# Optimization experiments

Measured on AMD Instinct MI355X. Metric: run time of the kernel, lower is better.

Reference implementation:

```python
import jax, jax.numpy as jnp
import numpy as np

N_EMBD = 1024
N_HEAD = 16
EPS = 1e-5


def setup_inputs() -> dict:
    key = jax.random.key(0)
    ks = jax.random.split(key, 12)
    C = N_EMBD
    s = 1.0 / np.sqrt(C)
    s4 = 1.0 / np.sqrt(4 * C)
    return {
        "x": jax.random.normal(ks[0], (2, 2048, C), jnp.float32),
        # attention projections (stored as [in, out])
        "wq": jax.random.normal(ks[1], (C, C), jnp.float32) * s,
        "bq": jnp.zeros((C,), jnp.float32),
        "wk": jax.random.normal(ks[2], (C, C), jnp.float32) * s,
        "bk": jnp.zeros((C,), jnp.float32),
        "wv": jax.random.normal(ks[3], (C, C), jnp.float32) * s,
        "bv": jnp.zeros((C,), jnp.float32),
        # layernorms
        "ln1_w": jnp.ones((C,), jnp.float32),
        "ln1_b": jnp.zeros((C,), jnp.float32),
        "ln2_w": jnp.ones((C,), jnp.float32),
        "ln2_b": jnp.zeros((C,), jnp.float32),
        # MLP
        "w_fc": jax.random.normal(ks[4], (C, 4 * C), jnp.float32) * s,
        "b_fc": jnp.zeros((4 * C,), jnp.float32),
        "w_proj": jax.random.normal(ks[5], (4 * C, C), jnp.float32) * s4,
        "b_proj": jnp.zeros((C,), jnp.float32),
    }


def _layer_norm(x, w, b):
    mu = jnp.mean(x, axis=-1, keepdims=True)
    var = jnp.var(x, axis=-1, keepdims=True)
    return (x - mu) * jax.lax.rsqrt(var + EPS) * w + b


def _block(x, wq, bq, wk, bk, wv, bv, ln1_w, ln1_b, ln2_w, ln2_b,
           w_fc, b_fc, w_proj, b_proj):
    B, T, C = x.shape
    H, D = N_HEAD, C // N_HEAD
    h = _layer_norm(x, ln1_w, ln1_b)
    q = (h @ wq + bq).reshape(B, T, H, D).transpose(0, 2, 1, 3)  # [B,H,T,D]
    k = (h @ wk + bk).reshape(B, T, H, D).transpose(0, 2, 1, 3)
    v = (h @ wv + bv).reshape(B, T, H, D).transpose(0, 2, 1, 3)
    att = jnp.einsum("bhtd,bhsd->bhts", q, k) / np.sqrt(D)
    causal = jnp.tril(jnp.ones((T, T), bool))
    att = jnp.where(causal, att, -jnp.inf)
    att = jax.nn.softmax(att, axis=-1)
    y = jnp.einsum("bhts,bhsd->bhtd", att, v)
    y = y.transpose(0, 2, 1, 3).reshape(B, T, C)
    x = x + y
    h2 = _layer_norm(x, ln2_w, ln2_b)
    mlp = jax.nn.gelu(h2 @ w_fc + b_fc, approximate=False) @ w_proj + b_proj
    x = x + mlp
    return x, k, v


def reference(x, wq, bq, wk, bk, wv, bv, ln1_w, ln1_b, ln2_w, ln2_b,
              w_fc, b_fc, w_proj, b_proj):
    return _block(x, wq, bq, wk, bk, wv, bv, ln1_w, ln1_b, ln2_w, ln2_b,
                  w_fc, b_fc, w_proj, b_proj)
```

## Files before the change

### kernel.cpp

```cpp
#include <hip/hip_runtime.h>
#include <hip/hip_bf16.h>


#define T_SEQ 2048
#define C_DIM 1024
#define HEADS 16
#define HD    64

typedef __attribute__((ext_vector_type(8))) short s16x8;
typedef __attribute__((ext_vector_type(4))) short s16x4;
typedef __attribute__((ext_vector_type(4))) float f32x4;

__device__ __forceinline__ short f2bf(float f) {
    union { __hip_bfloat16 h; short s; } u;
    u.h = __float2bfloat16(f);
    return u.s;
}
__device__ __forceinline__ float bf2f(short s) {
    union { float f; unsigned u; } u;
    u.u = ((unsigned)(unsigned short)s) << 16;
    return u.f;
}

__device__ __forceinline__ void gload16(const void* g, void* l) {
    __builtin_amdgcn_global_load_lds(
        (const __attribute__((address_space(1))) void*)g,
        (__attribute__((address_space(3))) void*)l, 16, 0, 0);
}
#define VMCNT0 asm volatile("s_waitcnt vmcnt(0)" ::: "memory")
#define PRIO1  __builtin_amdgcn_s_setprio(1)
#define PRIO0  __builtin_amdgcn_s_setprio(0)

__global__ __launch_bounds__(256) void prep_kernel(
    const float* __restrict__ wq, const float* __restrict__ wk, const float* __restrict__ wv,
    const float* __restrict__ wfc, const float* __restrict__ wpr,
    short* __restrict__ wqkvt, short* __restrict__ wfct, short* __restrict__ wprt,
    const float* __restrict__ x, const float* __restrict__ ln1w, const float* __restrict__ ln1b,
    short* __restrict__ hb) {
    int b = blockIdx.x, tid = threadIdx.x;
    if (b < 11264) {
        const float* W; short* Wt; int K, N, n0, k0;
        if (b < 3072) {
            int which = b >> 10, sub = b & 1023;
            W = (which == 0) ? wq : ((which == 1) ? wk : wv);
            Wt = wqkvt + which * 1024 * 1024;
            K = 1024; N = 1024;
            n0 = (sub & 31) * 32; k0 = (sub >> 5) * 32;
        } else if (b < 7168) {
            int sub = b - 3072;
            W = wfc; Wt = wfct; K = 1024; N = 4096;
            n0 = (sub & 127) * 32; k0 = (sub >> 7) * 32;
        } else {
            int sub = b - 7168;
            W = wpr; Wt = wprt; K = 4096; N = 1024;
            n0 = (sub & 31) * 32; k0 = (sub >> 5) * 32;
        }
        __shared__ float t[32][33];
        int ty = tid >> 3, tx = tid & 7;
        float4 v = *(const float4*)&W[(size_t)(k0 + ty) * N + n0 + tx * 4];
        t[ty][tx * 4 + 0] = v.x; t[ty][tx * 4 + 1] = v.y;
        t[ty][tx * 4 + 2] = v.z; t[ty][tx * 4 + 3] = v.w;
        __syncthreads();
        int r = tid >> 3, c = tid & 7;
        s16x4 o;
#pragma unroll
        for (int j = 0; j < 4; j++) o[j] = f2bf(t[c * 4 + j][r]);
        *(s16x4*)&Wt[(size_t)(n0 + r) * K + k0 + c * 4] = o;
    } else {
        int row = b - 11264;
        float4 v = ((const float4*)(x + (size_t)row * C_DIM))[tid];
        float s  = v.x + v.y + v.z + v.w;
        float sq = v.x * v.x + v.y * v.y + v.z * v.z + v.w * v.w;
#pragma unroll
        for (int off = 32; off > 0; off >>= 1) {
            s  += __shfl_down(s, off, 64);
            sq += __shfl_down(sq, off, 64);
        }
        __shared__ float rs[4], rq[4];
        int wv2 = tid >> 6, ln = tid & 63;
        if (ln == 0) { rs[wv2] = s; rq[wv2] = sq; }
        __syncthreads();
        s = rs[0] + rs[1] + rs[2] + rs[3];
        sq = rq[0] + rq[1] + rq[2] + rq[3];
        float mean = s * (1.f / C_DIM);
        float rstd = rsqrtf(sq * (1.f / C_DIM) - mean * mean + 1e-5f);
        float4 wv4 = ((const float4*)ln1w)[tid];
        float4 bv4 = ((const float4*)ln1b)[tid];
        s16x4 o;
        o[0] = f2bf((v.x - mean) * rstd * wv4.x + bv4.x);
        o[1] = f2bf((v.y - mean) * rstd * wv4.y + bv4.y);
        o[2] = f2bf((v.z - mean) * rstd * wv4.z + bv4.z);
        o[3] = f2bf((v.w - mean) * rstd * wv4.w + bv4.w);
        *(s16x4*)(hb + (size_t)row * C_DIM + tid * 4) = o;
    }
}

__global__ __launch_bounds__(256) void resln_kernel(
    const float* __restrict__ x, const float* __restrict__ y,
    const float* __restrict__ w, const float* __restrict__ b,
    const float* __restrict__ bproj,
    short* __restrict__ out, float* __restrict__ xout) {
    int row = blockIdx.x, tid = threadIdx.x;
    float4 vx = ((const float4*)(x + row * C_DIM))[tid];
    float4 vy = ((const float4*)(y + row * C_DIM))[tid];
    float4 v;
    v.x = vx.x + vy.x; v.y = vx.y + vy.y; v.z = vx.z + vy.z; v.w = vx.w + vy.w;
    float4 bp = ((const float4*)bproj)[tid];
    float4 xo;
    xo.x = v.x + bp.x; xo.y = v.y + bp.y; xo.z = v.z + bp.z; xo.w = v.w + bp.w;
    ((float4*)(xout + row * C_DIM))[tid] = xo;
    float s  = v.x + v.y + v.z + v.w;
    float sq = v.x * v.x + v.y * v.y + v.z * v.z + v.w * v.w;
#pragma unroll
    for (int off = 32; off > 0; off >>= 1) {
        s  += __shfl_down(s, off, 64);
        sq += __shfl_down(sq, off, 64);
    }
    __shared__ float rs[4], rq[4];
    int wv = tid >> 6, ln = tid & 63;
    if (ln == 0) { rs[wv] = s; rq[wv] = sq; }
    __syncthreads();
    s = rs[0] + rs[1] + rs[2] + rs[3];
    sq = rq[0] + rq[1] + rq[2] + rq[3];
    float mean = s * (1.f / C_DIM);
    float rstd = rsqrtf(sq * (1.f / C_DIM) - mean * mean + 1e-5f);
    float4 wv4 = ((const float4*)w)[tid];
    float4 bv4 = ((const float4*)b)[tid];
    s16x4 o;
    o[0] = f2bf((v.x - mean) * rstd * wv4.x + bv4.x);
    o[1] = f2bf((v.y - mean) * rstd * wv4.y + bv4.y);
    o[2] = f2bf((v.z - mean) * rstd * wv4.z + bv4.z);
    o[3] = f2bf((v.w - mean) * rstd * wv4.w + bv4.w);
    *(s16x4*)(out + row * C_DIM + tid * 4) = o;
}

__global__ __launch_bounds__(256) void reduce_kernel(
    const short* __restrict__ p, float* __restrict__ xout) {
    size_t i = (size_t)blockIdx.x * 256 + threadIdx.x;
    float4 a = ((const float4*)xout)[i];
#pragma unroll
    for (int c = 0; c < 4; c++) {
        s16x4 v = ((const s16x4*)(p + (size_t)c * 4194304))[i];
        a.x += bf2f(v[0]); a.y += bf2f(v[1]); a.z += bf2f(v[2]); a.w += bf2f(v[3]);
    }
    ((float4*)xout)[i] = a;
}

template<int MODE>
__global__ __launch_bounds__(512, 1) void gemm2p(
    const short* __restrict__ A, const short* __restrict__ Bt,
    int K, int LDA, int N,
    const float* __restrict__ b0, const float* __restrict__ b1, const float* __restrict__ b2,
    short* __restrict__ os0, short* __restrict__ os1, short* __restrict__ os2,
    float* __restrict__ of0) {
    constexpr int MFR = 8, NFR = 4;

    __shared__ short As[2][256 * 64];
    __shared__ short Bs[2][256 * 64];

    const int tid = threadIdx.x;
    const int wv = tid >> 6, lane = tid & 63, g = lane >> 4, r4 = lane & 15;
    const int wm = wv >> 2, wn = wv & 3;
    const int lr = lane >> 3, lc = lane & 7, sc = lc ^ lr;

    const int nwg = gridDim.x * gridDim.y;
    const int bid = blockIdx.y * gridDim.x + blockIdx.x;
    const int swz = (bid & 7) * (nwg >> 3) + (bid >> 3);
    const int m0 = (swz % gridDim.x) * 256;
    const int yy = swz / gridDim.x;
    int n0, kch;
    if constexpr (MODE == 2) {
        kch = yy >> 2;
        n0 = (yy & 3) * 256;
    } else {
        kch = 0;
        n0 = yy * 256;
    }
    const size_t kbase = (size_t)kch * K;
    const size_t aoff = (size_t)m0 * LDA + kbase + sc * 8;
    const size_t boff = (size_t)n0 * LDA + kbase + sc * 8;

    const f32x4 zero4 = {0.f, 0.f, 0.f, 0.f};
    f32x4 acc[MFR][NFR];
#pragma unroll
    for (int i = 0; i < MFR; i++)
#pragma unroll
        for (int j = 0; j < NFR; j++) acc[i][j] = zero4;

    auto stage = [&](int bb, int t1) {
#pragma unroll
        for (int j = 0; j < 4; j++) {
            int rbase = j * 64 + wv * 8;
            gload16(A  + aoff + (size_t)(rbase + lr) * LDA + (size_t)t1 * 64, &As[bb][rbase * 64]);
            gload16(Bt + boff + (size_t)(rbase + lr) * LDA + (size_t)t1 * 64, &Bs[bb][rbase * 64]);
        }
    };

    stage(0, 0);
    __syncthreads();

    const int NT = K >> 6;
    int cur = 0;
    for (int t = 0; t < NT; ++t) {
        if (t + 1 < NT) stage(cur ^ 1, t + 1);
        const char* Ac = (const char*)&As[cur][0];
        const char* Bc = (const char*)&Bs[cur][0];
#pragma unroll
        for (int kk = 0; kk < 2; kk++) {
            s16x8 aF[MFR], bF[NFR];
#pragma unroll
            for (int mf = 0; mf < MFR; mf++) {
                int row = wm * 128 + mf * 16 + r4;
                aF[mf] = *(const s16x8*)(Ac + ((row * 128 + kk * 64 + g * 16) ^ ((row & 7) << 4)));
            }
#pragma unroll
            for (int nf = 0; nf < NFR; nf++) {
                int row = wn * 64 + nf * 16 + r4;
                bF[nf] = *(const s16x8*)(Bc + ((row * 128 + kk * 64 + g * 16) ^ ((row & 7) << 4)));
            }
            PRIO1;
#pragma unroll
            for (int mf = 0; mf < MFR; mf++)
#pragma unroll
                for (int nf = 0; nf < NFR; nf++)
                    acc[mf][nf] = __builtin_amdgcn_mfma_f32_16x16x32_bf16(
                        aF[mf], bF[nf], acc[mf][nf], 0, 0, 0);
            PRIO0;
        }
        __syncthreads();
        cur ^= 1;
    }

#pragma unroll
    for (int mf = 0; mf < MFR; mf++) {
#pragma unroll
        for (int nf = 0; nf < NFR; nf++) {
            int n = n0 + wn * 64 + nf * 16 + r4;
            int mB = m0 + wm * 128 + mf * 16 + 4 * g;
            if constexpr (MODE == 0) {
                int sel = n >> 10, nn = n & 1023;
                const float* bp = (sel == 0) ? b0 : ((sel == 1) ? b1 : b2);
                float bias = bp[nn];
                int h = nn >> 6, d = nn & 63;
                int bb2 = mB >> 11, tt = mB & 2047;
                size_t qz = ((size_t)(bb2 * HEADS + h) * T_SEQ + tt) * HD + d;
                if (sel == 0) {
#pragma unroll
                    for (int r = 0; r < 4; r++)
                        os0[qz + (size_t)r * HD] = f2bf((acc[mf][nf][r] + bias) * 0.18033688f);
                } else if (sel == 1) {
#pragma unroll
                    for (int r = 0; r < 4; r++) {
                        float val = acc[mf][nf][r] + bias;
                        os1[qz + (size_t)r * HD] = f2bf(val);
                        of0[qz + (size_t)r * HD] = val;
                    }
                } else {
                    s16x4 vp;
#pragma unroll
                    for (int r = 0; r < 4; r++) {
                        float val = acc[mf][nf][r] + bias;
                        of0[4194304 + qz + (size_t)r * HD] = val;
                        vp[r] = f2bf(val);
                    }
                    *(s16x4*)&os2[((size_t)(bb2 * HEADS + h) * HD + d) * T_SEQ + tt] = vp;
                }
            } else if constexpr (MODE == 1) {
                float bias = b0[n];
#pragma unroll
                for (int r = 0; r < 4; r++) {
                    float val = acc[mf][nf][r] + bias;
                    float u = val * (0.7978845608f + 0.0356774081f * val * val);
                    float e = exp2f(fminf(u * 2.885390082f, 126.f));
                    val = val * e * (1.f / 1.f + 0.f);
                    val = (acc[mf][nf][r] + bias);
                    u = val * (0.7978845608f + 0.0356774081f * val * val);
                    e = exp2f(fminf(u * 2.885390082f, 126.f));
                    val = val * (e / (e + 1.f));
                    os0[(size_t)(mB + r) * N + n] = f2bf(val);
                }
            } else {
#pragma unroll
                for (int r = 0; r < 4; r++)
                    os0[(size_t)kch * 4194304 + (size_t)(mB + r) * N + n] = f2bf(acc[mf][nf][r]);
            }
        }
    }
}

__global__ __launch_bounds__(512) void attn_kernel(
    const short* __restrict__ qb, const short* __restrict__ kb,
    const short* __restrict__ vtb, float* __restrict__ y) {
    __shared__ short Ks[2][2][64 * 64];
    __shared__ short Vs[2][2][64 * 64];
    __shared__ short Ps[8][32 * 64];
    __shared__ float MLb[4][2][16][2];
    float* Ymrg = (float*)&Ps[0][0];

    int bx = blockIdx.x, bh = blockIdx.y;
    int tid = threadIdx.x, w = tid >> 6, lane = tid & 63, g = lane >> 4, r4 = lane & 15;
    int wq = w & 3, g2 = w >> 2;
    int lr = lane >> 3, lc = lane & 7, sc = lc ^ lr;
    const f32x4 zero4 = {0.f, 0.f, 0.f, 0.f};

    for (int ph = 0; ph < 2; ++ph) {
        int qtr = ph ? bx : (15 - bx);
        int qbase = qtr * 128;

        const short* Qp = qb + ((size_t)bh * T_SEQ + qbase + wq * 32 + r4) * HD;
        s16x8 qf[2][2];
        qf[0][0] = *(const s16x8*)&Qp[g * 8];
        qf[0][1] = *(const s16x8*)&Qp[32 + g * 8];
        qf[1][0] = *(const s16x8*)&Qp[16 * HD + g * 8];
        qf[1][1] = *(const s16x8*)&Qp[16 * HD + 32 + g * 8];

        f32x4 yacc[2][4];
#pragma unroll
        for (int qh = 0; qh < 2; qh++)
#pragma unroll
            for (int ni = 0; ni < 4; ni++) yacc[qh][ni] = zero4;
        float mrun[2] = {-1e30f, -1e30f}, lrun[2] = {0.f, 0.f};

#pragma unroll
        for (int j = 0; j < 2; j++) {
            int rw = (wq * 2 + j) * 8 + lr;
            gload16(kb  + ((size_t)bh * T_SEQ + g2 * 64 + rw) * HD + sc * 8,
                    &Ks[g2][0][(wq * 2 + j) * 512]);
            gload16(vtb + ((size_t)bh * HD + rw) * T_SEQ + g2 * 64 + sc * 8,
                    &Vs[g2][0][(wq * 2 + j) * 512]);
        }
        VMCNT0;
        __syncthreads();

        for (int i = 0; i <= qtr; ++i) {
            int cur = i & 1;
            int s0 = (2 * i + g2) * 64;
            if (i + 1 <= qtr) {
#pragma unroll
                for (int j = 0; j < 2; j++) {
                    int rw = (wq * 2 + j) * 8 + lr;
                    gload16(kb  + ((size_t)bh * T_SEQ + s0 + 128 + rw) * HD + sc * 8,
                            &Ks[g2][cur ^ 1][(wq * 2 + j) * 512]);
                    gload16(vtb + ((size_t)bh * HD + rw) * T_SEQ + s0 + 128 + sc * 8,
                            &Vs[g2][cur ^ 1][(wq * 2 + j) * 512]);
                }
            }
            f32x4 sacc[2][4];
#pragma unroll
            for (int qh = 0; qh < 2; qh++)
#pragma unroll
                for (int sb = 0; sb < 4; sb++) sacc[qh][sb] = zero4;
            PRIO1;
#pragma unroll
            for (int kk = 0; kk < 2; kk++) {
#pragma unroll
                for (int sb = 0; sb < 4; sb++) {
                    int srow = sb * 16 + r4;
                    s16x8 kf = *(const s16x8*)((const char*)&Ks[g2][cur][0] +
                                ((srow * 128 + kk * 64 + g * 16) ^ ((r4 & 7) << 4)));
                    sacc[0][sb] = __builtin_amdgcn_mfma_f32_16x16x32_bf16(kf, qf[0][kk], sacc[0][sb], 0, 0, 0);
                    sacc[1][sb] = __builtin_amdgcn_mfma_f32_16x16x32_bf16(kf, qf[1][kk], sacc[1][sb], 0, 0, 0);
                }
            }
            PRIO0;
            bool diag = (i == qtr);
            float p[2][4][4];
#pragma unroll
            for (int qh = 0; qh < 2; qh++) {
                float mx = -3e38f;
#pragma unroll
                for (int sb = 0; sb < 4; sb++)
#pragma unroll
                    for (int r = 0; r < 4; r++) {
                        float v = sacc[qh][sb][r];
                        if (diag) {
                            int kv = s0 + sb * 16 + 4 * g + r;
                            int qg = qbase + wq * 32 + qh * 16 + r4;
                            if (kv > qg) v = -3e38f;
                        }
                        p[qh][sb][r] = v;
                        mx = fmaxf(mx, v);
                    }
                mx = fmaxf(mx, __shfl_xor(mx, 16, 64));
                mx = fmaxf(mx, __shfl_xor(mx, 32, 64));
                if (!__all(mx <= mrun[qh] + 8.f)) {
                    float mnew = fmaxf(mrun[qh], mx);
                    float alpha = exp2f(mrun[qh] - mnew);
                    float aC[4];
#pragma unroll
                    for (int r = 0; r < 4; r++) aC[r] = __shfl(alpha, 4 * g + r, 64);
#pragma unroll
                    for (int ni = 0; ni < 4; ni++)
#pragma unroll
                        for (int r = 0; r < 4; r++) yacc[qh][ni][r] *= aC[r];
                    lrun[qh] *= alpha;
                    mrun[qh] = mnew;
                }
                float rsum = 0.f;
#pragma unroll
                for (int sb = 0; sb < 4; sb++)
#pragma unroll
                    for (int r = 0; r < 4; r++) {
                        float e = exp2f(p[qh][sb][r] - mrun[qh]);
                        p[qh][sb][r] = e;
                        rsum += e;
                    }
                rsum += __shfl_xor(rsum, 16, 64);
                rsum += __shfl_xor(rsum, 32, 64);
                lrun[qh] += rsum;
#pragma unroll
                for (int sb = 0; sb < 4; sb++) {
                    s16x4 pk;
#pragma unroll
                    for (int r = 0; r < 4; r++) pk[r] = f2bf(p[qh][sb][r]);
                    int off = (((qh * 16 + r4) * 128) + (sb * 16 + 4 * g) * 2) ^ ((r4 & 7) << 4);
                    *(s16x4*)((char*)&Ps[w][0] + off) = pk;
                }
            }
            PRIO1;
#pragma unroll
            for (int kk = 0; kk < 2; kk++) {
                s16x8 pf[2];
#pragma unroll
                for (int qh = 0; qh < 2; qh++)
                    pf[qh] = *(const s16x8*)((const char*)&Ps[w][0] +
                              ((((qh * 16 + r4) * 128) + kk * 64 + g * 16) ^ ((r4 & 7) << 4)));
#pragma unroll
                for (int ni = 0; ni < 4; ni++) {
                    int vrow = ni * 16 + r4;
                    s16x8 vb = *(const s16x8*)((const char*)&Vs[g2][cur][0] +
                                ((vrow * 128 + kk * 64 + g * 16) ^ ((r4 & 7) << 4)));
                    yacc[0][ni] = __builtin_amdgcn_mfma_f32_16x16x32_bf16(pf[0], vb, yacc[0][ni], 0, 0, 0);
                    yacc[1][ni] = __builtin_amdgcn_mfma_f32_16x16x32_bf16(pf[1], vb, yacc[1][ni], 0, 0, 0);
                }
            }
            PRIO0;
            VMCNT0;
            __syncthreads();
        }
        if (g2 == 1) {
            if (g == 0) {
#pragma unroll
                for (int qh = 0; qh < 2; qh++) {
                    MLb[wq][qh][r4][0] = mrun[qh];
                    MLb[wq][qh][r4][1] = lrun[qh];
                }
            }
#pragma unroll
            for (int qh = 0; qh < 2; qh++)
#pragma unroll
                for (int ni = 0; ni < 4; ni++)
#pragma unroll
                    for (int r = 0; r < 4; r++)
                        Ymrg[wq * 2048 + (qh * 16 + 4 * g + r) * 64 + ni * 16 + r4] = yacc[qh][ni][r];
        }
        __syncthreads();
        if (g2 == 0) {
            int bb = bh >> 4, h = bh & 15;
#pragma unroll
            for (int qh = 0; qh < 2; qh++) {
                float m_b = MLb[wq][qh][r4][0], l_b = MLb[wq][qh][r4][1];
                float mM = fmaxf(mrun[qh], m_b);
                float fa = exp2f(mrun[qh] - mM), fb = exp2f(m_b - mM);
                float lM = lrun[qh] * fa + l_b * fb;
                float faC[4], fbC[4], lC[4];
#pragma unroll
                for (int r = 0; r < 4; r++) {
                    faC[r] = __shfl(fa, 4 * g + r, 64);
                    fbC[r] = __shfl(fb, 4 * g + r, 64);
                    lC[r]  = __shfl(lM, 4 * g + r, 64);
                }
#pragma unroll
                for (int ni = 0; ni < 4; ni++)
#pragma unroll
                    for (int r = 0; r < 4; r++) {
                        float yv = yacc[qh][ni][r] * faC[r] +
                                   Ymrg[wq * 2048 + (qh * 16 + 4 * g + r) * 64 + ni * 16 + r4] * fbC[r];
                        int q = qbase + wq * 32 + qh * 16 + 4 * g + r;
                        y[((size_t)bb * T_SEQ + q) * C_DIM + h * HD + ni * 16 + r4] = yv / lC[r];
                    }
            }
        }
        __syncthreads();
    }
}

extern "C" void kernel_launch(void* const* d_in, const int* in_sizes, int n_in,
                              void* d_out, int out_size, void* d_ws, size_t ws_size,
                              hipStream_t stream) {
    (void)in_sizes; (void)n_in; (void)out_size; (void)ws_size;
    const float* x    = (const float*)d_in[0];
    const float* wq   = (const float*)d_in[1];
    const float* bq   = (const float*)d_in[2];
    const float* wk   = (const float*)d_in[3];
    const float* bk   = (const float*)d_in[4];
    const float* wvp  = (const float*)d_in[5];
    const float* bv   = (const float*)d_in[6];
    const float* ln1w = (const float*)d_in[7];
    const float* ln1b = (const float*)d_in[8];
    const float* ln2w = (const float*)d_in[9];
    const float* ln2b = (const float*)d_in[10];
    const float* wfc  = (const float*)d_in[11];
    const float* bfc  = (const float*)d_in[12];
    const float* wpr  = (const float*)d_in[13];
    const float* bpr  = (const float*)d_in[14];

    float* xout = (float*)d_out;
    float* kout = xout + 4194304;

    short* wqkvt = (short*)d_ws;
    short* wfct  = wqkvt + 3072 * 1024;
    short* wprt  = wfct + 4096 * 1024;
    short* hb    = wprt + 1024 * 4096;
    short* qb    = hb + 4096 * 1024;
    short* kbuf  = qb + 4096 * 1024;
    short* vtb   = kbuf + 4096 * 1024;
    short* h2b   = vtb + 4096 * 1024;
    short* fcb   = h2b + 4096 * 1024;
    float* ybuf  = (float*)(fcb + 4096 * 4096);
    short* pbuf  = qb;

    prep_kernel<<<15360, 256, 0, stream>>>(wq, wk, wvp, wfc, wpr,
        wqkvt, wfct, wprt, x, ln1w, ln1b, hb);

    gemm2p<0><<<dim3(16, 12), 512, 0, stream>>>(hb, wqkvt, 1024, 1024, 3072,
        bq, bk, bv, qb, kbuf, vtb, kout);

    attn_kernel<<<dim3(8, 32), 512, 0, stream>>>(qb, kbuf, vtb, ybuf);

    resln_kernel<<<4096, 256, 0, stream>>>(x, ybuf, ln2w, ln2b, bpr, h2b, xout);

    gemm2p<1><<<dim3(16, 16), 512, 0, stream>>>(h2b, wfct, 1024, 1024, 4096,
        bfc, nullptr, nullptr, fcb, nullptr, nullptr, nullptr);

    gemm2p<2><<<dim3(16, 16), 512, 0, stream>>>(fcb, wprt, 1024, 4096, 1024,
        nullptr, nullptr, nullptr, pbuf, nullptr, nullptr, nullptr);

    reduce_kernel<<<4096, 256, 0, stream>>>(pbuf, xout);
}
```

Before: 227.6 us.

## Single-buffer V tile and drop redundant GELU recomputation in MLP epilogue

In the attention kernel, V tiles are no longer double-buffered. V is loaded into a single buffer at the start of each iteration, and a partial vmcnt wait plus a barrier is placed between the softmax and the PV matmul. This shrinks shared memory from 80KB to 80KB-equivalent pool reuse (40960 shorts), which may allow more occupancy, at the cost of exposing V load latency behind QK^T and softmax only. The MLP epilogue also drops a duplicated GELU evaluation that was computed and then discarded.

```diff
diff --git a/kernel.cpp b/kernel.cpp
--- a/kernel.cpp
+++ b/kernel.cpp
@@ -30,6 +30,10 @@
 #define VMCNT0 asm volatile("s_waitcnt vmcnt(0)" ::: "memory")
 #define PRIO1  __builtin_amdgcn_s_setprio(1)
 #define PRIO0  __builtin_amdgcn_s_setprio(0)
+
+template<int N> __device__ __forceinline__ void vmcnt_n() {
+    asm volatile("s_waitcnt vmcnt(%0)" :: "n"(N) : "memory");
+}
 
 __global__ __launch_bounds__(256) void prep_kernel(
     const float* __restrict__ wq, const float* __restrict__ wk, const float* __restrict__ wv,
@@ -272,10 +276,6 @@
                     float val = acc[mf][nf][r] + bias;
                     float u = val * (0.7978845608f + 0.0356774081f * val * val);
                     float e = exp2f(fminf(u * 2.885390082f, 126.f));
-                    val = val * e * (1.f / 1.f + 0.f);
-                    val = (acc[mf][nf][r] + bias);
-                    u = val * (0.7978845608f + 0.0356774081f * val * val);
-                    e = exp2f(fminf(u * 2.885390082f, 126.f));
                     val = val * (e / (e + 1.f));
                     os0[(size_t)(mB + r) * N + n] = f2bf(val);
                 }
@@ -291,17 +291,20 @@
 __global__ __launch_bounds__(512) void attn_kernel(
     const short* __restrict__ qb, const short* __restrict__ kb,
     const short* __restrict__ vtb, float* __restrict__ y) {
-    __shared__ short Ks[2][2][64 * 64];
-    __shared__ short Vs[2][2][64 * 64];
-    __shared__ short Ps[8][32 * 64];
-    __shared__ float MLb[4][2][16][2];
-    float* Ymrg = (float*)&Ps[0][0];
-
+    __shared__ short pool[40960];
     int bx = blockIdx.x, bh = blockIdx.y;
     int tid = threadIdx.x, w = tid >> 6, lane = tid & 63, g = lane >> 4, r4 = lane & 15;
     int wq = w & 3, g2 = w >> 2;
     int lr = lane >> 3, lc = lane & 7, sc = lc ^ lr;
     const f32x4 zero4 = {0.f, 0.f, 0.f, 0.f};
+
+    short* Kb[2];
+    Kb[0] = pool + g2 * 8192;
+    Kb[1] = pool + g2 * 8192 + 4096;
+    short* Vb  = pool + 16384 + g2 * 4096;
+    short* Pw  = pool + 24576 + w * 2048;
+    float* Ymrg = (float*)(pool + 24576);
+    float* MLb  = (float*)(pool + 16384);
 
     for (int ph = 0; ph < 2; ++ph) {
         int qtr = ph ? bx : (15 - bx);
@@ -324,10 +327,8 @@
 #pragma unroll
         for (int j = 0; j < 2; j++) {
             int rw = (wq * 2 + j) * 8 + lr;
-            gload16(kb  + ((size_t)bh * T_SEQ + g2 * 64 + rw) * HD + sc * 8,
-                    &Ks[g2][0][(wq * 2 + j) * 512]);
-            gload16(vtb + ((size_t)bh * HD + rw) * T_SEQ + g2 * 64 + sc * 8,
-                    &Vs[g2][0][(wq * 2 + j) * 512]);
+            gload16(kb + ((size_t)bh * T_SEQ + g2 * 64 + rw) * HD + sc * 8,
+                    Kb[0] + (wq * 2 + j) * 512);
         }
         VMCNT0;
         __syncthreads();
@@ -335,14 +336,18 @@
         for (int i = 0; i <= qtr; ++i) {
             int cur = i & 1;
             int s0 = (2 * i + g2) * 64;
+#pragma unroll
+            for (int j = 0; j < 2; j++) {
+                int rw = (wq * 2 + j) * 8 + lr;
+                gload16(vtb + ((size_t)bh * HD + rw) * T_SEQ + s0 + sc * 8,
+                        Vb + (wq * 2 + j) * 512);
+            }
             if (i + 1 <= qtr) {
 #pragma unroll
                 for (int j = 0; j < 2; j++) {
                     int rw = (wq * 2 + j) * 8 + lr;
-                    gload16(kb  + ((size_t)bh * T_SEQ + s0 + 128 + rw) * HD + sc * 8,
-                            &Ks[g2][cur ^ 1][(wq * 2 + j) * 512]);
-                    gload16(vtb + ((size_t)bh * HD + rw) * T_SEQ + s0 + 128 + sc * 8,
-                            &Vs[g2][cur ^ 1][(wq * 2 + j) * 512]);
+                    gload16(kb + ((size_t)bh * T_SEQ + s0 + 128 + rw) * HD + sc * 8,
+                            Kb[cur ^ 1] + (wq * 2 + j) * 512);
                 }
             }
             f32x4 sacc[2][4];
@@ -356,7 +361,7 @@
 #pragma unroll
                 for (int sb = 0; sb < 4; sb++) {
                     int srow = sb * 16 + r4;
-                    s16x8 kf = *(const s16x8*)((const char*)&Ks[g2][cur][0] +
+                    s16x8 kf = *(const s16x8*)((const char*)Kb[cur] +
                                 ((srow * 128 + kk * 64 + g * 16) ^ ((r4 & 7) << 4)));
                     sacc[0][sb] = __builtin_amdgcn_mfma_f32_16x16x32_bf16(kf, qf[0][kk], sacc[0][sb], 0, 0, 0);
                     sacc[1][sb] = __builtin_amdgcn_mfma_f32_16x16x32_bf16(kf, qf[1][kk], sacc[1][sb], 0, 0, 0);
@@ -408,27 +413,31 @@
                 rsum += __shfl_xor(rsum, 16, 64);
                 rsum += __shfl_xor(rsum, 32, 64);
                 lrun[qh] += rsum;
+            }
+            if (i + 1 <= qtr) vmcnt_n<4>(); else vmcnt_n<0>();
+            __syncthreads();
+#pragma unroll
+            for (int qh = 0; qh < 2; qh++)
 #pragma unroll
                 for (int sb = 0; sb < 4; sb++) {
                     s16x4 pk;
 #pragma unroll
                     for (int r = 0; r < 4; r++) pk[r] = f2bf(p[qh][sb][r]);
                     int off = (((qh * 16 + r4) * 128) + (sb * 16 + 4 * g) * 2) ^ ((r4 & 7) << 4);
-                    *(s16x4*)((char*)&Ps[w][0] + off) = pk;
-                }
-            }
+                    *(s16x4*)((char*)Pw + off) = pk;
+                }
             PRIO1;
 #pragma unroll
             for (int kk = 0; kk < 2; kk++) {
                 s16x8 pf[2];
 #pragma unroll
                 for (int qh = 0; qh < 2; qh++)
-                    pf[qh] = *(const s16x8*)((const char*)&Ps[w][0] +
+                    pf[qh] = *(const s16x8*)((const char*)Pw +
                               ((((qh * 16 + r4) * 128) + kk * 64 + g * 16) ^ ((r4 & 7) << 4)));
 #pragma unroll
                 for (int ni = 0; ni < 4; ni++) {
                     int vrow = ni * 16 + r4;
-                    s16x8 vb = *(const s16x8*)((const char*)&Vs[g2][cur][0] +
+                    s16x8 vb = *(const s16x8*)((const char*)Vb +
                                 ((vrow * 128 + kk * 64 + g * 16) ^ ((r4 & 7) << 4)));
                     yacc[0][ni] = __builtin_amdgcn_mfma_f32_16x16x32_bf16(pf[0], vb, yacc[0][ni], 0, 0, 0);
                     yacc[1][ni] = __builtin_amdgcn_mfma_f32_16x16x32_bf16(pf[1], vb, yacc[1][ni], 0, 0, 0);
@@ -442,8 +451,8 @@
             if (g == 0) {
 #pragma unroll
                 for (int qh = 0; qh < 2; qh++) {
-                    MLb[wq][qh][r4][0] = mrun[qh];
-                    MLb[wq][qh][r4][1] = lrun[qh];
+                    MLb[((wq * 2 + qh) * 16 + r4) * 2 + 0] = mrun[qh];
+                    MLb[((wq * 2 + qh) * 16 + r4) * 2 + 1] = lrun[qh];
                 }
             }
 #pragma unroll
@@ -459,7 +468,8 @@
             int bb = bh >> 4, h = bh & 15;
 #pragma unroll
             for (int qh = 0; qh < 2; qh++) {
-                float m_b = MLb[wq][qh][r4][0], l_b = MLb[wq][qh][r4][1];
+                float m_b = MLb[((wq * 2 + qh) * 16 + r4) * 2 + 0];
+                float l_b = MLb[((wq * 2 + qh) * 16 + r4) * 2 + 1];
                 float mM = fmaxf(mrun[qh], m_b);
                 float fa = exp2f(mrun[qh] - mM), fb = exp2f(m_b - mM);
                 float lM = lrun[qh] * fa + l_b * fb;
```

After: 230.8 us. No clear change (+1.4%).
